# Kernel optimization log

Measured on AMD Instinct MI355X. Metric: run time of the kernel, lower is better.

The kernel has to match this reference:

```python
import jax, jax.numpy as jnp
import numpy as np

N_HEAD = 16
NEG = -1e10


def setup_inputs() -> dict:
    key = jax.random.key(0)
    ks = jax.random.split(key, 10)
    B, T, C = 2, 2048, 1024
    hs = C // N_HEAD
    inv = 1.0 / np.sqrt(C)
    return {
        "x": jax.random.normal(ks[0], (B, T, C), jnp.float32),
        "W1": jax.random.normal(ks[1], (C, C), jnp.float32) * inv,
        "bw1": jnp.zeros((C,), jnp.float32),
        "b1": jnp.zeros((hs,), jnp.float32),
        # original init: uniform(-0.001, 0.001)
        "w2": jax.random.uniform(ks[2], (hs, T), jnp.float32, -0.001, 0.001),
        "b2": jnp.zeros((T,), jnp.float32),
        "Wv": jax.random.normal(ks[3], (C, C), jnp.float32) * inv,
        "bv": jnp.zeros((C,), jnp.float32),
        "Wp": jax.random.normal(ks[4], (C, C), jnp.float32) * inv,
        "bp": jnp.zeros((C,), jnp.float32),
    }


def reference(x, W1, bw1, b1, w2, b2, Wv, bv, Wp, bp):
    B, T, C = x.shape
    nh = N_HEAD
    hs = C // nh
    # factorized synthesizer 'query': (B, nh, T, hs)
    h = (x @ W1 + bw1).reshape(B, T, nh, hs).transpose(0, 2, 1, 3)
    # scores: relu(h + b1) @ w2 + b2  -> (B, nh, T, T)
    att = jnp.einsum('bhtd,dk->bhtk', jax.nn.relu(h + b1), w2[:, :T]) + b2[:T]
    # causal mask then softmax (masked_fill with -1e10, as in original)
    causal = jnp.tril(jnp.ones((T, T), bool))
    att = jnp.where(causal[None, None], att, NEG)
    att = jax.nn.softmax(att, axis=-1)
    # values
    v = (x @ Wv + bv).reshape(B, T, nh, hs).transpose(0, 2, 1, 3)
    y = jnp.einsum('bhtk,bhkd->bhtd', att, v)
    y = y.transpose(0, 2, 1, 3).reshape(B, T, C)
    return y @ Wp + bp
```

## Files before the change

### kernel.cpp

```cpp
#include <hip/hip_runtime.h>
#include <hip/hip_bf16.h>

#define TSEQ 2048
#define CDIM 1024
#define NH 16
#define HS 64

typedef __attribute__((ext_vector_type(8))) short bf16x8;
typedef __attribute__((ext_vector_type(4))) float f32x4;
typedef __attribute__((ext_vector_type(16))) float f32x16;

__device__ inline void gload16(const void* g, void* l) {
    __builtin_amdgcn_global_load_lds((const __attribute__((address_space(1))) void*)g,
                                     (__attribute__((address_space(3))) void*)l, 16, 0, 0);
}

__device__ inline unsigned packbf(float a, float b) {
    union { __hip_bfloat162 h; unsigned u; } cv;
    cv.h = __float22bfloat162_rn(make_float2(a, b));
    return cv.u;
}

__global__ __launch_bounds__(256)
void conv_bf16(const float* __restrict__ in, __hip_bfloat16* __restrict__ out, int n) {
    int i = (blockIdx.x * 256 + threadIdx.x) * 4;
    if (i + 3 < n) {
        float4 v = *(const float4*)(in + i);
        union { ushort4 u; __hip_bfloat16 h[4]; } o;
        o.h[0] = __float2bfloat16(v.x);
        o.h[1] = __float2bfloat16(v.y);
        o.h[2] = __float2bfloat16(v.z);
        o.h[3] = __float2bfloat16(v.w);
        *(ushort4*)((unsigned short*)out + i) = o.u;
    }
}

__global__ __launch_bounds__(256)
void exp_b2(const float* __restrict__ b2, float* __restrict__ eb2, int n) {
    int i = blockIdx.x * 256 + threadIdx.x;
    if (i < n) eb2[i] = __expf(b2[i]);
}

__global__ __launch_bounds__(256)
void transpose_to_bf16(const float* __restrict__ in, __hip_bfloat16* __restrict__ out,
                       int R, int C) {
    __shared__ float t[32][33];
    const int tx = threadIdx.x & 31, ty = threadIdx.x >> 5;
    const int r0 = blockIdx.y * 32, c0 = blockIdx.x * 32;
    #pragma unroll
    for (int i = 0; i < 32; i += 8)
        t[ty + i][tx] = in[(size_t)(r0 + ty + i) * C + c0 + tx];
    __syncthreads();
    #pragma unroll
    for (int i = 0; i < 32; i += 8)
        out[(size_t)(c0 + ty + i) * R + r0 + tx] = __float2bfloat16(t[tx][ty + i]);
}

__global__ __launch_bounds__(256)
void transpose3_to_bf16(const float* __restrict__ W1, const float* __restrict__ Wv,
                        const float* __restrict__ Wp, __hip_bfloat16* __restrict__ o1,
                        __hip_bfloat16* __restrict__ o2, __hip_bfloat16* __restrict__ o3) {
    __shared__ float t[32][33];
    const float* in = blockIdx.z == 0 ? W1 : (blockIdx.z == 1 ? Wv : Wp);
    __hip_bfloat16* out = blockIdx.z == 0 ? o1 : (blockIdx.z == 1 ? o2 : o3);
    const int tx = threadIdx.x & 31, ty = threadIdx.x >> 5;
    const int r0 = blockIdx.y * 32, c0 = blockIdx.x * 32;
    #pragma unroll
    for (int i = 0; i < 32; i += 8)
        t[ty + i][tx] = in[(size_t)(r0 + ty + i) * CDIM + c0 + tx];
    __syncthreads();
    #pragma unroll
    for (int i = 0; i < 32; i += 8)
        out[(size_t)(c0 + ty + i) * CDIM + r0 + tx] = __float2bfloat16(t[tx][ty + i]);
}

__global__ __launch_bounds__(256, 2)
void gemm_qv(const __hip_bfloat16* __restrict__ X, const __hip_bfloat16* __restrict__ W,
             const float* __restrict__ bw1, const float* __restrict__ b1,
             const float* __restrict__ bv, __hip_bfloat16* __restrict__ Hb,
             __hip_bfloat16* __restrict__ Vblk, int M)
{
    __shared__ __align__(16) __hip_bfloat16 As[128 * 32];
    __shared__ __align__(16) __hip_bfloat16 Bs[128 * 32];
    const int tid = threadIdx.x, wave = tid >> 6, lane = tid & 63;
    const int wr = wave >> 1, wc = wave & 1, l15 = lane & 15, l4 = lane >> 4;
    const int m0 = blockIdx.y * 128, n0 = blockIdx.x * 128;
    const int K = CDIM;
    const int Bb = M >> 11;
    const int srow = wave * 32 + (lane >> 2), scol = (lane & 3) * 8;
    const __hip_bfloat16* xg = X + (size_t)(m0 + srow) * K + scol;
    const __hip_bfloat16* wg = W + (size_t)(n0 + srow) * K + scol;
    __hip_bfloat16* la = &As[wave * 32 * 32];
    __hip_bfloat16* lb = &Bs[wave * 32 * 32];

    f32x4 acc[4][4] = {};
    for (int k0 = 0; k0 < K; k0 += 32) {
        __syncthreads();
        gload16(xg + k0, la);
        gload16(xg + k0 + (size_t)16 * K, la + 16 * 32);
        gload16(wg + k0, lb);
        gload16(wg + k0 + (size_t)16 * K, lb + 16 * 32);
        __syncthreads();
        bf16x8 af[4], bfr[4];
        #pragma unroll
        for (int f = 0; f < 4; f++) af[f]  = *(const bf16x8*)&As[(wr * 64 + f * 16 + l15) * 32 + l4 * 8];
        #pragma unroll
        for (int f = 0; f < 4; f++) bfr[f] = *(const bf16x8*)&Bs[(wc * 64 + f * 16 + l15) * 32 + l4 * 8];
        #pragma unroll
        for (int fr = 0; fr < 4; fr++)
            #pragma unroll
            for (int fc = 0; fc < 4; fc++)
                acc[fr][fc] = __builtin_amdgcn_mfma_f32_16x16x32_bf16(af[fr], bfr[fc], acc[fr][fc], 0, 0, 0);
    }

    const bool isH = (n0 < CDIM);
    const int sl4 = ((l4 & 1) << 1) | (l4 >> 1);
    if (isH) {
        #pragma unroll
        for (int fc = 0; fc < 4; fc++) {
            const int col = n0 + wc * 64 + fc * 16 + l15;
            const float bias = bw1[col] + b1[col & (HS - 1)];
            #pragma unroll
            for (int fr = 0; fr < 4; fr++)
                #pragma unroll
                for (int r = 0; r < 4; r++) {
                    const int row = m0 + wr * 64 + fr * 16 + l4 * 4 + r;
                    const float hv = fmaxf(acc[fr][fc][r] + bias, 0.f) * 1.44269504f;
                    Hb[(size_t)row * CDIM + col] = __float2bfloat16(hv);
                }
        }
    } else {
        const int mt = m0 + wr * 64;
        const int bb = mt >> 11;
        const int ktb = (mt & (TSEQ - 1)) >> 6;
        const int hh = ((n0 - CDIM) + wc * 64) >> 6;
        __hip_bfloat16* tile = Vblk + (((size_t)hh * Bb + bb) * (TSEQ / 64) + ktb) * (HS * 64);
        #pragma unroll
        for (int fc = 0; fc < 4; fc++) {
            const int d = fc * 16 + l15;
            const int c2 = hh * HS + d;
            const float bias = bv[c2];
            #pragma unroll
            for (int fr = 0; fr < 4; fr++) {
                const int tl = fr * 16 + sl4 * 4;
                union { ushort4 u; __hip_bfloat16 h[4]; } o;
                #pragma unroll
                for (int r = 0; r < 4; r++) o.h[r] = __float2bfloat16(acc[fr][fc][r] + bias);
                *(ushort4*)(tile + (size_t)d * 64 + tl) = o.u;
            }
        }
    }
}

__global__ __launch_bounds__(256, 2)
void gemm_proj(const __hip_bfloat16* __restrict__ X, const __hip_bfloat16* __restrict__ Wt,
               const float* __restrict__ bN, float* __restrict__ Out, int M)
{
    __shared__ __align__(16) __hip_bfloat16 As[128 * 32];
    __shared__ __align__(16) __hip_bfloat16 Bs[128 * 32];
    const int tid = threadIdx.x, wave = tid >> 6, lane = tid & 63;
    const int wr = wave >> 1, wc = wave & 1, l15 = lane & 15, l4 = lane >> 4;
    const int m0 = blockIdx.y * 128, n0 = blockIdx.x * 128;
    const int K = CDIM;
    const int srow = wave * 32 + (lane >> 2), scol = (lane & 3) * 8;
    const __hip_bfloat16* xg = X + (size_t)(m0 + srow) * K + scol;
    const __hip_bfloat16* wg = Wt + (size_t)(n0 + srow) * K + scol;
    __hip_bfloat16* la = &As[wave * 32 * 32];
    __hip_bfloat16* lb = &Bs[wave * 32 * 32];

    f32x4 acc[4][4] = {};
    for (int k0 = 0; k0 < K; k0 += 32) {
        __syncthreads();
        gload16(xg + k0, la);
        gload16(xg + k0 + (size_t)16 * K, la + 16 * 32);
        gload16(wg + k0, lb);
        gload16(wg + k0 + (size_t)16 * K, lb + 16 * 32);
        __syncthreads();
        bf16x8 af[4], bfr[4];
        #pragma unroll
        for (int f = 0; f < 4; f++) af[f]  = *(const bf16x8*)&As[(wr * 64 + f * 16 + l15) * 32 + l4 * 8];
        #pragma unroll
        for (int f = 0; f < 4; f++) bfr[f] = *(const bf16x8*)&Bs[(wc * 64 + f * 16 + l15) * 32 + l4 * 8];
        #pragma unroll
        for (int fr = 0; fr < 4; fr++)
            #pragma unroll
            for (int fc = 0; fc < 4; fc++)
                acc[fr][fc] = __builtin_amdgcn_mfma_f32_16x16x32_bf16(af[fr], bfr[fc], acc[fr][fc], 0, 0, 0);
    }

    #pragma unroll
    for (int fc = 0; fc < 4; fc++) {
        const int col = n0 + wc * 64 + fc * 16 + l15;
        const float bias = bN[col];
        #pragma unroll
        for (int fr = 0; fr < 4; fr++)
            #pragma unroll
            for (int r = 0; r < 4; r++) {
                const int row = m0 + wr * 64 + fr * 16 + l4 * 4 + r;
                Out[(size_t)row * CDIM + col] = acc[fr][fc][r] + bias;
            }
    }
}

#define STAGEKV(KT, BUF) do {                                                   \
    gload16(kg0 + (size_t)(KT) * (64 * HS), &Ks[BUF][(w * 16) * 64]);           \
    gload16(kg1 + (size_t)(KT) * (64 * HS), &Ks[BUF][(w * 16 + 8) * 64]);       \
    gload16(vg0 + (size_t)(KT) * (HS * 64), &Vs[BUF][(w * 16) * 64]);           \
    gload16(vg1 + (size_t)(KT) * (HS * 64), &Vs[BUF][(w * 16 + 8) * 64]);       \
} while (0)

__global__ __launch_bounds__(256, 2)
void attn_mfma12(const __hip_bfloat16* __restrict__ H, const __hip_bfloat16* __restrict__ w2t,
                 const __hip_bfloat16* __restrict__ Vblk, const float* __restrict__ eb2,
                 __hip_bfloat16* __restrict__ Y, int M)
{
    __shared__ __align__(16) __hip_bfloat16 Ks[2][64 * 64];
    __shared__ __align__(16) __hip_bfloat16 Vs[2][64 * 64];
    __shared__ float Ls[4 * 32];

    const int tid = threadIdx.x;
    const int w = tid >> 6, lane = tid & 63;
    const int l31 = lane & 31, hi = lane >> 5;
    const int h = blockIdx.y, b = blockIdx.z;
    const int u = (blockIdx.x + blockIdx.y) & 15;
    const int qb = b ? (15 - u) : u;
    const int q0 = qb * 128;
    const int qw = q0 + w * 32;
    const int swz = l31 & 7;
    const int Bb = M >> 11;

    const int srr = lane >> 3, spc = lane & 7;
    const int sr0 = w * 16 + srr, sr1 = sr0 + 8;
    const int sc = (spc ^ srr) * 8;
    const __hip_bfloat16* kg0 = w2t + (size_t)sr0 * HS + sc;
    const __hip_bfloat16* kg1 = w2t + (size_t)sr1 * HS + sc;
    const __hip_bfloat16* vpan = Vblk + (((size_t)h * Bb + b) * (TSEQ / 64)) * (HS * 64);
    const __hip_bfloat16* vg0 = vpan + (size_t)sr0 * 64 + sc;
    const __hip_bfloat16* vg1 = vpan + (size_t)sr1 * 64 + sc;

    bf16x8 hf[4];
    {
        const size_t row = (size_t)(b * TSEQ + qw + l31);
        #pragma unroll
        for (int kk = 0; kk < 4; kk++)
            hf[kk] = *(const bf16x8*)(H + row * CDIM + h * HS + kk * 16 + hi * 8);
    }

    f32x16 yacc[2] = {};
    float lsum = 0.f;
    const int ntile = 2 * qb + 2;

    STAGEKV(0, 0);
    __syncthreads();

    int cur = 0;
    for (int kt = 0; kt < ntile; kt++) {
        const int k0 = kt * 64;
        if (kt + 1 < ntile) STAGEKV(kt + 1, cur ^ 1);
        if (k0 <= qw + 31) {
            const bool nomask = (k0 + 63 <= qw);
            bf16x8 pa[4];
            #pragma unroll
            for (int tf = 0; tf < 2; tf++) {
                float4 eb[4];
                #pragma unroll
                for (int g = 0; g < 4; g++)
                    eb[g] = *(const float4*)(eb2 + k0 + tf * 32 + g * 8 + hi * 4);
                f32x16 st = {};
                #pragma unroll
                for (int kk = 0; kk < 4; kk++) {
                    const int cs = (kk * 2 + hi) ^ swz;
                    bf16x8 kf = *(const bf16x8*)((const char*)&Ks[cur][0] + (tf * 32 + l31) * 128 + cs * 16);
                    st = __builtin_amdgcn_mfma_f32_32x32x16_bf16(kf, hf[kk], st, 0, 0, 0);
                }
                const int qg = qw + l31;
                float p[16];
                #pragma unroll
                for (int r = 0; r < 16; r++) {
                    float e = __builtin_amdgcn_exp2f(st[r]) * ((const float*)&eb[r >> 2])[r & 3];
                    if (!nomask) {
                        const int tg = k0 + tf * 32 + (r & 3) + 8 * (r >> 2) + 4 * hi;
                        if (tg > qg) e = 0.f;
                    }
                    p[r] = e;
                    lsum += e;
                }
                #pragma unroll
                for (int m = 0; m < 2; m++) {
                    union { unsigned d[4]; bf16x8 v; } pk;
                    #pragma unroll
                    for (int dw = 0; dw < 4; dw++)
                        pk.d[dw] = packbf(p[8 * m + 2 * dw], p[8 * m + 2 * dw + 1]);
                    pa[tf * 2 + m] = pk.v;
                }
            }
            #pragma unroll
            for (int ks = 0; ks < 4; ks++) {
                const int cs = (ks * 2 + hi) ^ swz;
                #pragma unroll
                for (int df = 0; df < 2; df++) {
                    bf16x8 vf = *(const bf16x8*)((const char*)&Vs[cur][0] + (df * 32 + l31) * 128 + cs * 16);
                    yacc[df] = __builtin_amdgcn_mfma_f32_32x32x16_bf16(pa[ks], vf, yacc[df], 0, 0, 0);
                }
            }
        }
        __syncthreads();
        cur ^= 1;
    }

    lsum += __shfl_xor(lsum, 32);
    if (hi == 0) Ls[w * 32 + l31] = lsum;
    __syncthreads();

    #pragma unroll
    for (int g = 0; g < 4; g++) {
        float4 lv = *(const float4*)&Ls[w * 32 + g * 8 + hi * 4];
        #pragma unroll
        for (int df = 0; df < 2; df++)
            #pragma unroll
            for (int rr = 0; rr < 4; rr++) {
                const float v = yacc[df][g * 4 + rr] / ((const float*)&lv)[rr];
                const size_t row = (size_t)(b * TSEQ + qw + 8 * g + 4 * hi + rr);
                Y[row * CDIM + h * HS + df * 32 + l31] = __float2bfloat16(v);
            }
    }
}

extern "C" void kernel_launch(void* const* d_in, const int* in_sizes, int n_in,
                              void* d_out, int out_size, void* d_ws, size_t ws_size,
                              hipStream_t stream) {
    const float* x   = (const float*)d_in[0];
    const float* W1  = (const float*)d_in[1];
    const float* bw1 = (const float*)d_in[2];
    const float* b1  = (const float*)d_in[3];
    const float* w2  = (const float*)d_in[4];
    const float* b2  = (const float*)d_in[5];
    const float* Wv  = (const float*)d_in[6];
    const float* bv  = (const float*)d_in[7];
    const float* Wp  = (const float*)d_in[8];
    const float* bp  = (const float*)d_in[9];
    float* out = (float*)d_out;

    const int B = in_sizes[0] / (TSEQ * CDIM);
    const int M = B * TSEQ;
    const size_t MC = (size_t)M * CDIM;
    const size_t WC = (size_t)CDIM * CDIM;

    __hip_bfloat16* xb  = (__hip_bfloat16*)d_ws;
    __hip_bfloat16* Wqv = xb  + MC;
    __hip_bfloat16* Wpt = Wqv + 2 * WC;
    __hip_bfloat16* w2t = Wpt + WC;
    __hip_bfloat16* Hb  = w2t + (size_t)TSEQ * HS;
    __hip_bfloat16* Vbk = Hb  + MC;
    __hip_bfloat16* Yb  = Vbk + MC;
    float*          eb2 = (float*)(Yb + MC);

    dim3 blk(256);
    conv_bf16<<<dim3((unsigned)(MC / 1024)), blk, 0, stream>>>(x, xb, (int)MC);
    exp_b2<<<dim3(TSEQ / 256), blk, 0, stream>>>(b2, eb2, TSEQ);
    transpose3_to_bf16<<<dim3(32, 32, 3), blk, 0, stream>>>(W1, Wv, Wp, Wqv, Wqv + WC, Wpt);
    transpose_to_bf16<<<dim3(TSEQ / 32, HS / 32), blk, 0, stream>>>(w2, w2t, HS, TSEQ);

    gemm_qv<<<dim3(16, M / 128), blk, 0, stream>>>(xb, Wqv, bw1, b1, bv, Hb, Vbk, M);

    attn_mfma12<<<dim3(16, NH, B), blk, 0, stream>>>(Hb, w2t, Vbk, eb2, Yb, M);

    gemm_proj<<<dim3(8, M / 128), blk, 0, stream>>>(Yb, Wpt, bp, out, M);
}
```

Before: 137.3 us.

## Triple-buffer K/V tiles, stage b2 bias in LDS, fold bias into MFMA accumulator

The attention kernel moves from double to triple buffering of the K/V tiles. It waits with explicit vmcnt counts and one raw barrier per iteration instead of two __syncthreads, so loads run two tiles ahead. The b2 bias is now pre-scaled by log2e and preloaded into LDS. It seeds the score accumulator, which removes a per-element multiply and the global loads of eb2. The cost is more LDS per block (about 56KB), which may limit residency to fewer than 2 blocks per CU, plus fragile hand-counted vmcnt waits.

Result: faster. 122.4 us (-10.8%).

```diff
diff --git a/kernel.cpp b/kernel.cpp
--- a/kernel.cpp
+++ b/kernel.cpp
@@ -36,9 +36,9 @@
 }
 
 __global__ __launch_bounds__(256)
-void exp_b2(const float* __restrict__ b2, float* __restrict__ eb2, int n) {
+void b2_log2e(const float* __restrict__ b2, float* __restrict__ bl, int n) {
     int i = blockIdx.x * 256 + threadIdx.x;
-    if (i < n) eb2[i] = __expf(b2[i]);
+    if (i < n) bl[i] = b2[i] * 1.44269504f;
 }
 
 __global__ __launch_bounds__(256)
@@ -210,12 +210,13 @@
 } while (0)
 
 __global__ __launch_bounds__(256, 2)
-void attn_mfma12(const __hip_bfloat16* __restrict__ H, const __hip_bfloat16* __restrict__ w2t,
-                 const __hip_bfloat16* __restrict__ Vblk, const float* __restrict__ eb2,
+void attn_mfma13(const __hip_bfloat16* __restrict__ H, const __hip_bfloat16* __restrict__ w2t,
+                 const __hip_bfloat16* __restrict__ Vblk, const float* __restrict__ bl,
                  __hip_bfloat16* __restrict__ Y, int M)
 {
-    __shared__ __align__(16) __hip_bfloat16 Ks[2][64 * 64];
-    __shared__ __align__(16) __hip_bfloat16 Vs[2][64 * 64];
+    __shared__ __align__(16) __hip_bfloat16 Ks[3][64 * 64];
+    __shared__ __align__(16) __hip_bfloat16 Vs[3][64 * 64];
+    __shared__ __align__(16) float bls[TSEQ];
     __shared__ float Ls[4 * 32];
 
     const int tid = threadIdx.x;
@@ -238,6 +239,9 @@
     const __hip_bfloat16* vg0 = vpan + (size_t)sr0 * 64 + sc;
     const __hip_bfloat16* vg1 = vpan + (size_t)sr1 * 64 + sc;
 
+    gload16(bl + (size_t)(w * 64 + lane) * 4 - (size_t)lane * 4 + (size_t)lane * 4, &bls[w * 256]);
+    gload16(bl + 1024 + (size_t)w * 256 + lane * 4 - (size_t)lane * 4 + (size_t)lane * 4, &bls[1024 + w * 256]);
+
     bf16x8 hf[4];
     {
         const size_t row = (size_t)(b * TSEQ + qw + l31);
@@ -251,33 +255,39 @@
     const int ntile = 2 * qb + 2;
 
     STAGEKV(0, 0);
-    __syncthreads();
-
-    int cur = 0;
+    STAGEKV(1, 1);
+
     for (int kt = 0; kt < ntile; kt++) {
         const int k0 = kt * 64;
-        if (kt + 1 < ntile) STAGEKV(kt + 1, cur ^ 1);
+        if (kt + 1 < ntile) asm volatile("s_waitcnt vmcnt(4)" ::: "memory");
+        else                asm volatile("s_waitcnt vmcnt(0)" ::: "memory");
+        __builtin_amdgcn_s_barrier();
+        __builtin_amdgcn_sched_barrier(0);
+        if (kt + 2 < ntile) STAGEKV(kt + 2, (kt + 2) % 3);
         if (k0 <= qw + 31) {
+            const int buf = kt % 3;
             const bool nomask = (k0 + 63 <= qw);
             bf16x8 pa[4];
             #pragma unroll
             for (int tf = 0; tf < 2; tf++) {
-                float4 eb[4];
-                #pragma unroll
-                for (int g = 0; g < 4; g++)
-                    eb[g] = *(const float4*)(eb2 + k0 + tf * 32 + g * 8 + hi * 4);
-                f32x16 st = {};
+                f32x16 st;
+                #pragma unroll
+                for (int g = 0; g < 4; g++) {
+                    float4 blv = *(const float4*)&bls[k0 + tf * 32 + g * 8 + hi * 4];
+                    st[g * 4 + 0] = blv.x; st[g * 4 + 1] = blv.y;
+                    st[g * 4 + 2] = blv.z; st[g * 4 + 3] = blv.w;
+                }
                 #pragma unroll
                 for (int kk = 0; kk < 4; kk++) {
                     const int cs = (kk * 2 + hi) ^ swz;
-                    bf16x8 kf = *(const bf16x8*)((const char*)&Ks[cur][0] + (tf * 32 + l31) * 128 + cs * 16);
+                    bf16x8 kf = *(const bf16x8*)((const char*)&Ks[buf][0] + (tf * 32 + l31) * 128 + cs * 16);
                     st = __builtin_amdgcn_mfma_f32_32x32x16_bf16(kf, hf[kk], st, 0, 0, 0);
                 }
                 const int qg = qw + l31;
                 float p[16];
                 #pragma unroll
                 for (int r = 0; r < 16; r++) {
-                    float e = __builtin_amdgcn_exp2f(st[r]) * ((const float*)&eb[r >> 2])[r & 3];
+                    float e = __builtin_amdgcn_exp2f(st[r]);
                     if (!nomask) {
                         const int tg = k0 + tf * 32 + (r & 3) + 8 * (r >> 2) + 4 * hi;
                         if (tg > qg) e = 0.f;
@@ -299,14 +309,13 @@
                 const int cs = (ks * 2 + hi) ^ swz;
                 #pragma unroll
                 for (int df = 0; df < 2; df++) {
-                    bf16x8 vf = *(const bf16x8*)((const char*)&Vs[cur][0] + (df * 32 + l31) * 128 + cs * 16);
+                    bf16x8 vf = *(const bf16x8*)((const char*)&Vs[buf][0] + (df * 32 + l31) * 128 + cs * 16);
                     yacc[df] = __builtin_amdgcn_mfma_f32_32x32x16_bf16(pa[ks], vf, yacc[df], 0, 0, 0);
                 }
             }
         }
-        __syncthreads();
-        cur ^= 1;
-    }
+    }
+    __syncthreads();
 
     lsum += __shfl_xor(lsum, 32);
     if (hi == 0) Ls[w * 32 + l31] = lsum;
@@ -353,17 +362,17 @@
     __hip_bfloat16* Hb  = w2t + (size_t)TSEQ * HS;
     __hip_bfloat16* Vbk = Hb  + MC;
     __hip_bfloat16* Yb  = Vbk + MC;
-    float*          eb2 = (float*)(Yb + MC);
+    float*          bl  = (float*)(Yb + MC);
 
     dim3 blk(256);
     conv_bf16<<<dim3((unsigned)(MC / 1024)), blk, 0, stream>>>(x, xb, (int)MC);
-    exp_b2<<<dim3(TSEQ / 256), blk, 0, stream>>>(b2, eb2, TSEQ);
+    b2_log2e<<<dim3(TSEQ / 256), blk, 0, stream>>>(b2, bl, TSEQ);
     transpose3_to_bf16<<<dim3(32, 32, 3), blk, 0, stream>>>(W1, Wv, Wp, Wqv, Wqv + WC, Wpt);
     transpose_to_bf16<<<dim3(TSEQ / 32, HS / 32), blk, 0, stream>>>(w2, w2t, HS, TSEQ);
 
     gemm_qv<<<dim3(16, M / 128), blk, 0, stream>>>(xb, Wqv, bw1, b1, bv, Hb, Vbk, M);
 
-    attn_mfma12<<<dim3(16, NH, B), blk, 0, stream>>>(Hb, w2t, Vbk, eb2, Yb, M);
+    attn_mfma13<<<dim3(16, NH, B), blk, 0, stream>>>(Hb, w2t, Vbk, bl, Yb, M);
 
     gemm_proj<<<dim3(8, M / 128), blk, 0, stream>>>(Yb, Wpt, bp, out, M);
 }
```
